# Kernel optimization log

Hardware: AMD Instinct MI355X
Metric: run time of the kernel (lower is better)

Reference implementation:

```python
import jax, jax.numpy as jnp
import numpy as np

N = 100_000      # num_nodes
E = 1_600_000    # num_edges (avg degree 16)
D = 64           # embedding_dim
L = 3            # num_layers


def setup_inputs() -> dict:
    key = jax.random.key(0)
    k1, k2 = jax.random.split(key)
    edge_index = jax.random.randint(k1, (2, E), 0, N, dtype=jnp.int64)
    edge_weight = jnp.ones((E,), jnp.float32)
    # nn.init.normal_(std=0.1)
    embedding = 0.1 * jax.random.normal(k2, (N, D), dtype=jnp.float32)
    return {"embedding": embedding, "edge_weight": edge_weight, "edge_index": edge_index}


def reference(embedding, edge_weight, edge_index):
    n = embedding.shape[0]
    self_idx = jnp.arange(n, dtype=edge_index.dtype)
    # add_self_loops: append (i, i) with weight 1 (PyG default fill_value)
    row = jnp.concatenate([edge_index[0], self_idx])  # source j
    col = jnp.concatenate([edge_index[1], self_idx])  # target i
    ew = jnp.concatenate([edge_weight, jnp.ones((n,), embedding.dtype)])
    # degree() counts occurrences of row (unweighted)
    deg = jax.ops.segment_sum(jnp.ones_like(ew), row, num_segments=n)
    deg_inv_sqrt = jnp.where(deg > 0, jax.lax.rsqrt(deg), 0.0)
    norm = deg_inv_sqrt[row] * ew * deg_inv_sqrt[col]  # [E+N]

    x = embedding
    acc = embedding  # running sum of layer-0..L embeddings
    for _ in range(L):
        # gather from source, scale, scatter-add to target (dropout off in eval)
        msg = norm[:, None] * x[row]                       # [E+N, D]
        x = jax.ops.segment_sum(msg, col, num_segments=n)  # [N, D]
        acc = acc + x
    return acc / (L + 1)
```

## Files before the change

### kernel.cpp

```cpp
#include <hip/hip_runtime.h>
#include <stdint.h>

#define DIM 64
#define BINS2 50000
#define RANGES 2
#define NSLICE 64
#define TBH 1024
#define SCAN_TILE 1024

__device__ __forceinline__ unsigned bf16rne(float f) {
    unsigned u = __float_as_uint(f);
    return (u + 0x7FFFu + ((u >> 16) & 1u)) >> 16;
}
__device__ __forceinline__ unsigned pack2(float lo, float hi) {
    return bf16rne(lo) | (bf16rne(hi) << 16);
}
#define UNPK(u, lo, hi) { lo = __uint_as_float((u) << 16); hi = __uint_as_float((u) & 0xFFFF0000u); }

__global__ void __launch_bounds__(TBH)
hist_kernel(const int* __restrict__ src, const int* __restrict__ dst,
            unsigned short* __restrict__ partialsA, unsigned short* __restrict__ partialsB,
            unsigned short* __restrict__ lrank, int E, int N, int Es) {
    __shared__ unsigned h32[BINS2 / 2];
    const int b = blockIdx.x;
    const int kind = b / (RANGES * NSLICE);
    const int rs = b % (RANGES * NSLICE);
    const int r = rs / NSLICE, s = rs % NSLICE;
    const int base = r * BINS2;
    const int hi = min(base + BINS2, N);
    const int nbw = (hi - base + 1) >> 1;
    for (int j = threadIdx.x; j < nbw; j += TBH) h32[j] = 0;
    __syncthreads();
    const int e0 = s * Es, e1 = min(e0 + Es, E);
    if (kind == 0) {
#pragma unroll 4
        for (int i = e0 + threadIdx.x; i < e1; i += TBH) {
            unsigned j = (unsigned)(dst[i] - base);
            if (j < (unsigned)BINS2) {
                const unsigned sh = (j & 1) * 16;
                unsigned old = atomicAdd(&h32[j >> 1], 1u << sh);
                lrank[i] = (unsigned short)((old >> sh) & 0xFFFFu);
            }
        }
    } else {
#pragma unroll 4
        for (int i = e0 + threadIdx.x; i < e1; i += TBH) {
            unsigned j = (unsigned)(src[i] - base);
            if (j < (unsigned)BINS2) atomicAdd(&h32[j >> 1], 1u << ((j & 1) * 16));
        }
    }
    __syncthreads();
    unsigned* part = (unsigned*)((kind ? partialsB : partialsA) + (size_t)s * N + base);
    for (int j = threadIdx.x; j < nbw; j += TBH) part[j] = h32[j];
}

__global__ void __launch_bounds__(256)
merge_kernel(unsigned short* __restrict__ partialsA, const unsigned short* __restrict__ partialsB,
             int* __restrict__ indeg, float* __restrict__ dis, int N) {
    const int i = blockIdx.x * blockDim.x + threadIdx.x;
    if (i >= N) return;
    int run = 0;
    for (int s = 0; s < NSLICE; ++s) {
        int v = partialsA[(size_t)s * N + i];
        partialsA[(size_t)s * N + i] = (unsigned short)run;
        run += v;
    }
    indeg[i] = run;
    int od = 0;
    for (int s = 0; s < NSLICE; ++s) od += partialsB[(size_t)s * N + i];
    dis[i] = rsqrtf((float)od + 1.0f);
}


__global__ void __launch_bounds__(256)
scan_partial(const int* __restrict__ indeg, int* __restrict__ partial, int n) {
    __shared__ int wsum[4];
    const int tid = threadIdx.x;
    const int base = blockIdx.x * SCAN_TILE + tid * 4;
    int s = 0;
    if (base + 3 < n) {
        int4 v = *(const int4*)(indeg + base);
        s = v.x + v.y + v.z + v.w;
    } else {
        for (int i = 0; i < 4; ++i) if (base + i < n) s += indeg[base + i];
    }
    for (int off = 32; off > 0; off >>= 1) s += __shfl_down(s, off, 64);
    const int lane = tid & 63, wid = tid >> 6;
    if (lane == 0) wsum[wid] = s;
    __syncthreads();
    if (tid == 0) partial[blockIdx.x] = wsum[0] + wsum[1] + wsum[2] + wsum[3];
}

__global__ void scan_blocksums(int* __restrict__ partial, int* __restrict__ offsets,
                               int nblocks, int n) {
    __shared__ int buf[1024];
    const int t = threadIdx.x;
    int v = (t < nblocks) ? partial[t] : 0;
    buf[t] = v;
    __syncthreads();
    for (int off = 1; off < 1024; off <<= 1) {
        int add = (t >= off) ? buf[t - off] : 0;
        __syncthreads();
        buf[t] += add;
        __syncthreads();
    }
    if (t < nblocks) partial[t] = buf[t] - v;
    if (t == 1023) offsets[n] = buf[1023];
}

__global__ void __launch_bounds__(256)
scan_final(const int* __restrict__ indeg, const int* __restrict__ partial,
           int* __restrict__ offsets, int n) {
    __shared__ int wpre[4];
    const int tid = threadIdx.x;
    const int base = blockIdx.x * SCAN_TILE + tid * 4;
    int v0 = 0, v1 = 0, v2 = 0, v3 = 0;
    if (base + 3 < n) {
        int4 v = *(const int4*)(indeg + base);
        v0 = v.x; v1 = v.y; v2 = v.z; v3 = v.w;
    } else {
        if (base + 0 < n) v0 = indeg[base + 0];
        if (base + 1 < n) v1 = indeg[base + 1];
        if (base + 2 < n) v2 = indeg[base + 2];
        if (base + 3 < n) v3 = indeg[base + 3];
    }
    const int s = v0 + v1 + v2 + v3;
    int inc = s;
    const int lane = tid & 63, wid = tid >> 6;
    for (int off = 1; off < 64; off <<= 1) {
        int t = __shfl_up(inc, off, 64);
        if (lane >= off) inc += t;
    }
    if (lane == 63) wpre[wid] = inc;
    __syncthreads();
    if (tid == 0) {
        int r = 0;
        for (int w = 0; w < 4; ++w) { int t = wpre[w]; wpre[w] = r; r += t; }
    }
    __syncthreads();
    int run = (inc - s) + wpre[wid] + partial[blockIdx.x];
    if (base + 0 < n) { offsets[base + 0] = run; run += v0; }
    if (base + 1 < n) { offsets[base + 1] = run; run += v1; }
    if (base + 2 < n) { offsets[base + 2] = run; run += v2; }
    if (base + 3 < n) { offsets[base + 3] = run; run += v3; }
}

__global__ void __launch_bounds__(256)
fill_kernel(const int* __restrict__ src, const int* __restrict__ dst,
            const float* __restrict__ ew, const float* __restrict__ dis,
            const int* __restrict__ offsets, const unsigned short* __restrict__ sliceoff,
            const unsigned short* __restrict__ lrank, int2* __restrict__ csr,
            int E, int N, int Es) {
    const int i0 = (blockIdx.x * blockDim.x + threadIdx.x) * 4;
    if (i0 + 3 < E) {
        int4   ss = *(const int4*)(src + i0);
        int4   tt = *(const int4*)(dst + i0);
        float4 ww = *(const float4*)(ew + i0);
        ushort4 lr = *(const ushort4*)(lrank + i0);
        int sl = i0 / Es;
#define DO(K, SF, TF, WF, LF) { int sE = (i0 + K) / Es; \
        int slot = offsets[TF] + sliceoff[(size_t)sE * N + TF] + (int)(LF); \
        csr[slot] = make_int2(SF, __float_as_int(dis[SF] * (WF) * dis[TF])); }
        (void)sl;
        DO(0, ss.x, tt.x, ww.x, lr.x)
        DO(1, ss.y, tt.y, ww.y, lr.y)
        DO(2, ss.z, tt.z, ww.z, lr.z)
        DO(3, ss.w, tt.w, ww.w, lr.w)
#undef DO
    } else {
        for (int i = i0; i < E; ++i) {
            int sE = i / Es;
            int t = dst[i], sc = src[i];
            float w = dis[sc] * ew[i] * dis[t];
            int slot = offsets[t] + sliceoff[(size_t)sE * N + t] + (int)lrank[i];
            csr[slot] = make_int2(sc, __float_as_int(w));
        }
    }
}

__global__ void __launch_bounds__(256)
conv_kernel(const float4* __restrict__ in4, uint4* __restrict__ outb, int n8) {
    int i = blockIdx.x * blockDim.x + threadIdx.x;
    if (i >= n8) return;
    float4 a = in4[2 * i], b = in4[2 * i + 1];
    uint4 o;
    o.x = pack2(a.x, a.y); o.y = pack2(a.z, a.w);
    o.z = pack2(b.x, b.y); o.w = pack2(b.z, b.w);
    outb[i] = o;
}

__global__ void __launch_bounds__(256)
prop_kernel(const uint4* __restrict__ xg, const float4* __restrict__ emb4,
            uint4* __restrict__ xstore, float4* __restrict__ out4,
            const int* __restrict__ offsets, const int2* __restrict__ csr,
            const float* __restrict__ dis, int n, int mode) {
    const int lane = threadIdx.x & 63;
    const int fl  = lane & 7;
    const int sub = lane >> 3;
    const int wave = blockIdx.x * (blockDim.x >> 6) + (threadIdx.x >> 6);
    const int node = wave * 8 + sub;
    if (node >= n) return;

    const int beg = offsets[node];
    const int end = offsets[node + 1];
    const float d = dis[node];
    const float dd = d * d;

    float a0, a1, a2, a3, a4, a5, a6, a7;
    float4 s0, s1;
    if (mode == 0) {
        s0 = emb4[node * 16 + fl * 2];
        s1 = emb4[node * 16 + fl * 2 + 1];
        a0 = dd * s0.x; a1 = dd * s0.y; a2 = dd * s0.z; a3 = dd * s0.w;
        a4 = dd * s1.x; a5 = dd * s1.y; a6 = dd * s1.z; a7 = dd * s1.w;
    } else {
        uint4 q = xg[(size_t)node * 8 + fl];
        float l, h;
        UNPK(q.x, l, h) a0 = dd * l; a1 = dd * h;
        UNPK(q.y, l, h) a2 = dd * l; a3 = dd * h;
        UNPK(q.z, l, h) a4 = dd * l; a5 = dd * h;
        UNPK(q.w, l, h) a6 = dd * l; a7 = dd * h;
    }

#define EDGE(E, Q) { float w_ = __int_as_float((E).y); float l, h; \
    UNPK((Q).x, l, h) a0 = fmaf(w_, l, a0); a1 = fmaf(w_, h, a1); \
    UNPK((Q).y, l, h) a2 = fmaf(w_, l, a2); a3 = fmaf(w_, h, a3); \
    UNPK((Q).z, l, h) a4 = fmaf(w_, l, a4); a5 = fmaf(w_, h, a5); \
    UNPK((Q).w, l, h) a6 = fmaf(w_, l, a6); a7 = fmaf(w_, h, a7); }

    int p = beg;
    for (; p + 4 <= end; p += 4) {
        int2 e0 = csr[p + 0], e1 = csr[p + 1], e2 = csr[p + 2], e3 = csr[p + 3];
        uint4 q0 = xg[(size_t)e0.x * 8 + fl];
        uint4 q1 = xg[(size_t)e1.x * 8 + fl];
        uint4 q2 = xg[(size_t)e2.x * 8 + fl];
        uint4 q3 = xg[(size_t)e3.x * 8 + fl];
        EDGE(e0, q0) EDGE(e1, q1) EDGE(e2, q2) EDGE(e3, q3)
    }
    for (; p < end; ++p) {
        int2 e = csr[p];
        uint4 q = xg[(size_t)e.x * 8 + fl];
        EDGE(e, q)
    }
#undef EDGE

    if (mode != 2) {
        uint4 o;
        o.x = pack2(a0, a1); o.y = pack2(a2, a3);
        o.z = pack2(a4, a5); o.w = pack2(a6, a7);
        xstore[(size_t)node * 8 + fl] = o;
    }
    const int oi = node * 16 + fl * 2;
    if (mode == 0) {
        out4[oi]     = make_float4(0.25f * (s0.x + a0), 0.25f * (s0.y + a1),
                                   0.25f * (s0.z + a2), 0.25f * (s0.w + a3));
        out4[oi + 1] = make_float4(0.25f * (s1.x + a4), 0.25f * (s1.y + a5),
                                   0.25f * (s1.z + a6), 0.25f * (s1.w + a7));
    } else {
        float4 p0 = out4[oi], p1 = out4[oi + 1];
        out4[oi]     = make_float4(fmaf(0.25f, a0, p0.x), fmaf(0.25f, a1, p0.y),
                                   fmaf(0.25f, a2, p0.z), fmaf(0.25f, a3, p0.w));
        out4[oi + 1] = make_float4(fmaf(0.25f, a4, p1.x), fmaf(0.25f, a5, p1.y),
                                   fmaf(0.25f, a6, p1.z), fmaf(0.25f, a7, p1.w));
    }
}


extern "C" void kernel_launch(void* const* d_in, const int* in_sizes, int n_in,
                              void* d_out, int out_size, void* d_ws, size_t ws_size,
                              hipStream_t stream) {
    const float* emb = (const float*)d_in[0];
    const float* ew  = (const float*)d_in[1];
    const int*   ei  = (const int*)d_in[2];
    const int E = in_sizes[2] / 2;
    const int N = in_sizes[0] / DIM;
    const int* src = ei;
    const int* dst = ei + E;
    float* out = (float*)d_out;

    const int Es = (E + NSLICE - 1) / NSLICE;
    const int nscan = (N + SCAN_TILE - 1) / SCAN_TILE;

    char* w = (char*)d_ws;
    unsigned short* partialsA = (unsigned short*)w; w += (size_t)NSLICE * N * 2;
    size_t unionSz = (size_t)NSLICE * N * 2;
    size_t xbSz = (size_t)N * DIM * 2;
    if (xbSz > unionSz) unionSz = xbSz;
    unionSz = (unionSz + 255) & ~(size_t)255;
    unsigned short* partialsB = (unsigned short*)w;
    uint4* xb = (uint4*)w; w += unionSz;
    unsigned short* lrank = (unsigned short*)w; w += (size_t)E * 2;
    int* indeg   = (int*)w;  w += (size_t)N * 4;
    int* offsets = (int*)w;  w += (size_t)(N + 1) * 4;
    float* dis   = (float*)w; w += (size_t)N * 4;
    int* partial = (int*)w;  w += (size_t)1024 * 4;
    w = (char*)(((uintptr_t)w + 255) & ~(uintptr_t)255);
    int2* csr    = (int2*)w; w += (size_t)E * 8;
    w = (char*)(((uintptr_t)w + 255) & ~(uintptr_t)255);
    uint4* x0c   = (uint4*)w; w += (size_t)N * DIM * 2;
    uint4* xa    = (uint4*)w; w += (size_t)N * DIM * 2;

    const int TB = 256;
    hist_kernel<<<2 * RANGES * NSLICE, TBH, 0, stream>>>(src, dst, partialsA, partialsB,
                                                         lrank, E, N, Es);
    merge_kernel<<<(N + TB - 1) / TB, TB, 0, stream>>>(partialsA, partialsB,
                                                       indeg, dis, N);
    scan_partial<<<nscan, TB, 0, stream>>>(indeg, partial, N);
    scan_blocksums<<<1, 1024, 0, stream>>>(partial, offsets, nscan, N);
    scan_final<<<nscan, TB, 0, stream>>>(indeg, partial, offsets, N);
    const int e4 = (E + 3) / 4;
    fill_kernel<<<(e4 + TB - 1) / TB, TB, 0, stream>>>(src, dst, ew, dis, offsets,
                                                       partialsA, lrank, csr, E, N, Es);
    const int n8 = N * DIM / 8;
    conv_kernel<<<(n8 + TB - 1) / TB, TB, 0, stream>>>((const float4*)emb, x0c, n8);

    dim3 grid((N + 31) / 32), block(TB);
    prop_kernel<<<grid, block, 0, stream>>>(x0c, (const float4*)emb, xa, (float4*)out,
                                            offsets, csr, dis, N, 0);
    prop_kernel<<<grid, block, 0, stream>>>(xa, nullptr, xb, (float4*)out,
                                            offsets, csr, dis, N, 1);
    prop_kernel<<<grid, block, 0, stream>>>(xb, nullptr, nullptr, (float4*)out,
                                            offsets, csr, dis, N, 2);
}
```

Before: 285.3 us.

## Replace direct CSR scatter with two-pass radix partition by destination range

The single fill kernel, which scattered each edge straight to its CSR slot through random offsets and sliceoff lookups, is replaced by a coarse partition pass. Edges are counted per destination range (2048 nodes) per edge slice, scanned, and written into a 16-byte-per-edge staging buffer grouped by range. A place kernel then writes CSR entries range by range, so offset, sliceoff and csr accesses stay local to a small node window and cache better. The cost is extra kernel launches, a serial single-block scan, and an extra read and write of the 16-byte staging buffer, which shares workspace memory with the bf16 feature buffers.

Result: slower. 303.3 us (+6.3%).

```diff
diff --git a/kernel.cpp b/kernel.cpp
--- a/kernel.cpp
+++ b/kernel.cpp
@@ -7,6 +7,9 @@
 #define NSLICE 64
 #define TBH 1024
 #define SCAN_TILE 1024
+#define PSLICE 256
+#define RSHIFT 11
+#define PB_G 8
 
 __device__ __forceinline__ unsigned bf16rne(float f) {
     unsigned u = __float_as_uint(f);
@@ -145,36 +148,74 @@
     if (base + 3 < n) { offsets[base + 3] = run; run += v3; }
 }
 
-__global__ void __launch_bounds__(256)
-fill_kernel(const int* __restrict__ src, const int* __restrict__ dst,
-            const float* __restrict__ ew, const float* __restrict__ dis,
-            const int* __restrict__ offsets, const unsigned short* __restrict__ sliceoff,
-            const unsigned short* __restrict__ lrank, int2* __restrict__ csr,
-            int E, int N, int Es) {
-    const int i0 = (blockIdx.x * blockDim.x + threadIdx.x) * 4;
-    if (i0 + 3 < E) {
-        int4   ss = *(const int4*)(src + i0);
-        int4   tt = *(const int4*)(dst + i0);
-        float4 ww = *(const float4*)(ew + i0);
-        ushort4 lr = *(const ushort4*)(lrank + i0);
-        int sl = i0 / Es;
-#define DO(K, SF, TF, WF, LF) { int sE = (i0 + K) / Es; \
-        int slot = offsets[TF] + sliceoff[(size_t)sE * N + TF] + (int)(LF); \
-        csr[slot] = make_int2(SF, __float_as_int(dis[SF] * (WF) * dis[TF])); }
-        (void)sl;
-        DO(0, ss.x, tt.x, ww.x, lr.x)
-        DO(1, ss.y, tt.y, ww.y, lr.y)
-        DO(2, ss.z, tt.z, ww.z, lr.z)
-        DO(3, ss.w, tt.w, ww.w, lr.w)
-#undef DO
-    } else {
-        for (int i = i0; i < E; ++i) {
-            int sE = i / Es;
-            int t = dst[i], sc = src[i];
-            float w = dis[sc] * ew[i] * dis[t];
-            int slot = offsets[t] + sliceoff[(size_t)sE * N + t] + (int)lrank[i];
-            csr[slot] = make_int2(sc, __float_as_int(w));
-        }
+
+__global__ void __launch_bounds__(256)
+count_part(const int* __restrict__ dst, int* __restrict__ cnt, int E, int Esp, int NR) {
+    __shared__ int c[64];
+    const int p = blockIdx.x;
+    if (threadIdx.x < 64) c[threadIdx.x] = 0;
+    __syncthreads();
+    const int e0 = p * Esp, e1 = min(e0 + Esp, E);
+    for (int i = e0 + threadIdx.x; i < e1; i += 256)
+        atomicAdd(&c[dst[i] >> RSHIFT], 1);
+    __syncthreads();
+    if (threadIdx.x < NR) cnt[threadIdx.x * PSLICE + p] = c[threadIdx.x];
+}
+
+__global__ void scan_part(const int* __restrict__ cnt, int* __restrict__ pscan, int n) {
+    __shared__ int buf[1024];
+    const int t = threadIdx.x;
+    const int chunk = (n + 1023) / 1024;
+    const int b0 = t * chunk, b1 = min(b0 + chunk, n);
+    int s = 0;
+    for (int i = b0; i < b1; ++i) s += cnt[i];
+    buf[t] = s;
+    __syncthreads();
+    for (int off = 1; off < 1024; off <<= 1) {
+        int add = (t >= off) ? buf[t - off] : 0;
+        __syncthreads();
+        buf[t] += add;
+        __syncthreads();
+    }
+    int run = buf[t] - s;
+    for (int i = b0; i < b1; ++i) { pscan[i] = run; run += cnt[i]; }
+    if (t == 1023) pscan[n] = buf[1023];
+}
+
+__global__ void __launch_bounds__(256)
+part_kernel(const int* __restrict__ src, const int* __restrict__ dst,
+            const float* __restrict__ ew, const unsigned short* __restrict__ lrank,
+            const float* __restrict__ dis, const int* __restrict__ pscan,
+            int4* __restrict__ part, int E, int Esp, int Esh, int NR) {
+    __shared__ int cur[64];
+    const int p = blockIdx.x;
+    if (threadIdx.x < NR) cur[threadIdx.x] = pscan[threadIdx.x * PSLICE + p];
+    __syncthreads();
+    const int e0 = p * Esp, e1 = min(e0 + Esp, E);
+    for (int i = e0 + threadIdx.x; i < e1; i += 256) {
+        int t = dst[i], sc = src[i];
+        float w = dis[sc] * ew[i] * dis[t];
+        int sh = i / Esh;
+        int pos = atomicAdd(&cur[t >> RSHIFT], 1);
+        part[pos] = make_int4(sc, t, __float_as_int(w), (sh << 24) | (int)lrank[i]);
+    }
+}
+
+__global__ void __launch_bounds__(256)
+place_kernel(const int4* __restrict__ part, const int* __restrict__ pscan,
+             const int* __restrict__ offsets, const unsigned short* __restrict__ sliceoff,
+             int2* __restrict__ csr, int N) {
+    const int r = blockIdx.x / PB_G;
+    const int g = blockIdx.x % PB_G;
+    const int idx0 = r * PSLICE + g * (PSLICE / PB_G);
+    const int start = pscan[idx0];
+    const int end = pscan[idx0 + PSLICE / PB_G];
+    for (int j = start + threadIdx.x; j < end; j += 256) {
+        int4 e = part[j];
+        int sh = ((unsigned)e.w) >> 24;
+        int lr = e.w & 0x00FFFFFF;
+        int slot = offsets[e.y] + sliceoff[(size_t)sh * N + e.y] + lr;
+        csr[slot] = make_int2(e.x, e.z);
     }
 }
 
@@ -278,7 +319,9 @@
     const int* dst = ei + E;
     float* out = (float*)d_out;
 
-    const int Es = (E + NSLICE - 1) / NSLICE;
+    const int Esh = (E + NSLICE - 1) / NSLICE;
+    const int Esp = (E + PSLICE - 1) / PSLICE;
+    const int NR  = (N + (1 << RSHIFT) - 1) >> RSHIFT;
     const int nscan = (N + SCAN_TILE - 1) / SCAN_TILE;
 
     char* w = (char*)d_ws;
@@ -294,23 +337,35 @@
     int* offsets = (int*)w;  w += (size_t)(N + 1) * 4;
     float* dis   = (float*)w; w += (size_t)N * 4;
     int* partial = (int*)w;  w += (size_t)1024 * 4;
+    int* cnt     = (int*)w;  w += (size_t)64 * PSLICE * 4;
+    int* pscan   = (int*)w;  w += ((size_t)64 * PSLICE + 1) * 4;
     w = (char*)(((uintptr_t)w + 255) & ~(uintptr_t)255);
     int2* csr    = (int2*)w; w += (size_t)E * 8;
     w = (char*)(((uintptr_t)w + 255) & ~(uintptr_t)255);
-    uint4* x0c   = (uint4*)w; w += (size_t)N * DIM * 2;
-    uint4* xa    = (uint4*)w; w += (size_t)N * DIM * 2;
+    size_t xSz = (size_t)N * DIM * 2;
+    size_t partSz = (size_t)E * 16;
+    size_t bigSz = (2 * xSz > partSz) ? 2 * xSz : partSz;
+    int4*  part  = (int4*)w;
+    uint4* x0c   = (uint4*)w;
+    uint4* xa    = (uint4*)(w + xSz);
+    w += (bigSz + 255) & ~(size_t)255;
 
     const int TB = 256;
     hist_kernel<<<2 * RANGES * NSLICE, TBH, 0, stream>>>(src, dst, partialsA, partialsB,
-                                                         lrank, E, N, Es);
+                                                         lrank, E, N, Esh);
     merge_kernel<<<(N + TB - 1) / TB, TB, 0, stream>>>(partialsA, partialsB,
                                                        indeg, dis, N);
     scan_partial<<<nscan, TB, 0, stream>>>(indeg, partial, N);
     scan_blocksums<<<1, 1024, 0, stream>>>(partial, offsets, nscan, N);
     scan_final<<<nscan, TB, 0, stream>>>(indeg, partial, offsets, N);
-    const int e4 = (E + 3) / 4;
-    fill_kernel<<<(e4 + TB - 1) / TB, TB, 0, stream>>>(src, dst, ew, dis, offsets,
-                                                       partialsA, lrank, csr, E, N, Es);
+
+    count_part<<<PSLICE, TB, 0, stream>>>(dst, cnt, E, Esp, NR);
+    scan_part<<<1, 1024, 0, stream>>>(cnt, pscan, NR * PSLICE);
+    part_kernel<<<PSLICE, TB, 0, stream>>>(src, dst, ew, lrank, dis, pscan,
+                                           part, E, Esp, Esh, NR);
+    place_kernel<<<NR * PB_G, TB, 0, stream>>>(part, pscan, offsets, partialsA,
+                                               csr, N);
+
     const int n8 = N * DIM / 8;
     conv_kernel<<<(n8 + TB - 1) / TB, TB, 0, stream>>>((const float4*)emb, x0c, n8);
 
```

## Defer output accumulation to a combine kernel and unroll edge gathers by eight

Applied to the files above, without the earlier changes.

Each propagation layer now only writes its bf16 result. A new combine kernel sums the fp32 embedding and the three bf16 layer outputs into the final output. This replaces the per-layer fp32 read-modify-write of the output buffer with one pass, at the cost of an extra launch and storing a third bf16 layer buffer (xc, aliased with the histogram partials). The neighbor gather loop also gains an 8-wide unrolled stage to keep more loads in flight, which adds register pressure.

Measured after the change: 284.8 us. Within noise of the previous version (-0.2%).

```diff
diff --git a/kernel.cpp b/kernel.cpp
--- a/kernel.cpp
+++ b/kernel.cpp
@@ -157,11 +157,9 @@
         int4   tt = *(const int4*)(dst + i0);
         float4 ww = *(const float4*)(ew + i0);
         ushort4 lr = *(const ushort4*)(lrank + i0);
-        int sl = i0 / Es;
 #define DO(K, SF, TF, WF, LF) { int sE = (i0 + K) / Es; \
         int slot = offsets[TF] + sliceoff[(size_t)sE * N + TF] + (int)(LF); \
         csr[slot] = make_int2(SF, __float_as_int(dis[SF] * (WF) * dis[TF])); }
-        (void)sl;
         DO(0, ss.x, tt.x, ww.x, lr.x)
         DO(1, ss.y, tt.y, ww.y, lr.y)
         DO(2, ss.z, tt.z, ww.z, lr.z)
@@ -190,10 +188,10 @@
 }
 
 __global__ void __launch_bounds__(256)
-prop_kernel(const uint4* __restrict__ xg, const float4* __restrict__ emb4,
-            uint4* __restrict__ xstore, float4* __restrict__ out4,
+prop_kernel(const uint4* __restrict__ xg, const float4* __restrict__ selfF,
+            uint4* __restrict__ xstore,
             const int* __restrict__ offsets, const int2* __restrict__ csr,
-            const float* __restrict__ dis, int n, int mode) {
+            const float* __restrict__ dis, int n) {
     const int lane = threadIdx.x & 63;
     const int fl  = lane & 7;
     const int sub = lane >> 3;
@@ -207,10 +205,9 @@
     const float dd = d * d;
 
     float a0, a1, a2, a3, a4, a5, a6, a7;
-    float4 s0, s1;
-    if (mode == 0) {
-        s0 = emb4[node * 16 + fl * 2];
-        s1 = emb4[node * 16 + fl * 2 + 1];
+    if (selfF) {
+        float4 s0 = selfF[node * 16 + fl * 2];
+        float4 s1 = selfF[node * 16 + fl * 2 + 1];
         a0 = dd * s0.x; a1 = dd * s0.y; a2 = dd * s0.z; a3 = dd * s0.w;
         a4 = dd * s1.x; a5 = dd * s1.y; a6 = dd * s1.z; a7 = dd * s1.w;
     } else {
@@ -229,6 +226,20 @@
     UNPK((Q).w, l, h) a6 = fmaf(w_, l, a6); a7 = fmaf(w_, h, a7); }
 
     int p = beg;
+    for (; p + 8 <= end; p += 8) {
+        int2 e0 = csr[p + 0], e1 = csr[p + 1], e2 = csr[p + 2], e3 = csr[p + 3];
+        int2 e4 = csr[p + 4], e5 = csr[p + 5], e6 = csr[p + 6], e7 = csr[p + 7];
+        uint4 q0 = xg[(size_t)e0.x * 8 + fl];
+        uint4 q1 = xg[(size_t)e1.x * 8 + fl];
+        uint4 q2 = xg[(size_t)e2.x * 8 + fl];
+        uint4 q3 = xg[(size_t)e3.x * 8 + fl];
+        uint4 q4 = xg[(size_t)e4.x * 8 + fl];
+        uint4 q5 = xg[(size_t)e5.x * 8 + fl];
+        uint4 q6 = xg[(size_t)e6.x * 8 + fl];
+        uint4 q7 = xg[(size_t)e7.x * 8 + fl];
+        EDGE(e0, q0) EDGE(e1, q1) EDGE(e2, q2) EDGE(e3, q3)
+        EDGE(e4, q4) EDGE(e5, q5) EDGE(e6, q6) EDGE(e7, q7)
+    }
     for (; p + 4 <= end; p += 4) {
         int2 e0 = csr[p + 0], e1 = csr[p + 1], e2 = csr[p + 2], e3 = csr[p + 3];
         uint4 q0 = xg[(size_t)e0.x * 8 + fl];
@@ -244,25 +255,36 @@
     }
 #undef EDGE
 
-    if (mode != 2) {
-        uint4 o;
-        o.x = pack2(a0, a1); o.y = pack2(a2, a3);
-        o.z = pack2(a4, a5); o.w = pack2(a6, a7);
-        xstore[(size_t)node * 8 + fl] = o;
-    }
-    const int oi = node * 16 + fl * 2;
-    if (mode == 0) {
-        out4[oi]     = make_float4(0.25f * (s0.x + a0), 0.25f * (s0.y + a1),
-                                   0.25f * (s0.z + a2), 0.25f * (s0.w + a3));
-        out4[oi + 1] = make_float4(0.25f * (s1.x + a4), 0.25f * (s1.y + a5),
-                                   0.25f * (s1.z + a6), 0.25f * (s1.w + a7));
-    } else {
-        float4 p0 = out4[oi], p1 = out4[oi + 1];
-        out4[oi]     = make_float4(fmaf(0.25f, a0, p0.x), fmaf(0.25f, a1, p0.y),
-                                   fmaf(0.25f, a2, p0.z), fmaf(0.25f, a3, p0.w));
-        out4[oi + 1] = make_float4(fmaf(0.25f, a4, p1.x), fmaf(0.25f, a5, p1.y),
-                                   fmaf(0.25f, a6, p1.z), fmaf(0.25f, a7, p1.w));
-    }
+    uint4 o;
+    o.x = pack2(a0, a1); o.y = pack2(a2, a3);
+    o.z = pack2(a4, a5); o.w = pack2(a6, a7);
+    xstore[(size_t)node * 8 + fl] = o;
+}
+
+__global__ void __launch_bounds__(256)
+combine_kernel(const float4* __restrict__ emb4, const uint4* __restrict__ xa,
+               const uint4* __restrict__ xb, const uint4* __restrict__ xc,
+               float4* __restrict__ out4, int n8) {
+    int i = blockIdx.x * blockDim.x + threadIdx.x;
+    if (i >= n8) return;
+    float4 e0 = emb4[2 * i], e1 = emb4[2 * i + 1];
+    uint4 qa = xa[i], qb = xb[i], qc = xc[i];
+    float r[8] = { e0.x, e0.y, e0.z, e0.w, e1.x, e1.y, e1.z, e1.w };
+    float l, h;
+    UNPK(qa.x, l, h) r[0] += l; r[1] += h;
+    UNPK(qa.y, l, h) r[2] += l; r[3] += h;
+    UNPK(qa.z, l, h) r[4] += l; r[5] += h;
+    UNPK(qa.w, l, h) r[6] += l; r[7] += h;
+    UNPK(qb.x, l, h) r[0] += l; r[1] += h;
+    UNPK(qb.y, l, h) r[2] += l; r[3] += h;
+    UNPK(qb.z, l, h) r[4] += l; r[5] += h;
+    UNPK(qb.w, l, h) r[6] += l; r[7] += h;
+    UNPK(qc.x, l, h) r[0] += l; r[1] += h;
+    UNPK(qc.y, l, h) r[2] += l; r[3] += h;
+    UNPK(qc.z, l, h) r[4] += l; r[5] += h;
+    UNPK(qc.w, l, h) r[6] += l; r[7] += h;
+    out4[2 * i]     = make_float4(0.25f * r[0], 0.25f * r[1], 0.25f * r[2], 0.25f * r[3]);
+    out4[2 * i + 1] = make_float4(0.25f * r[4], 0.25f * r[5], 0.25f * r[6], 0.25f * r[7]);
 }
 
 
@@ -282,13 +304,13 @@
     const int nscan = (N + SCAN_TILE - 1) / SCAN_TILE;
 
     char* w = (char*)d_ws;
-    unsigned short* partialsA = (unsigned short*)w; w += (size_t)NSLICE * N * 2;
-    size_t unionSz = (size_t)NSLICE * N * 2;
-    size_t xbSz = (size_t)N * DIM * 2;
-    if (xbSz > unionSz) unionSz = xbSz;
-    unionSz = (unionSz + 255) & ~(size_t)255;
+    size_t partSz = ((size_t)NSLICE * N * 2 + 255) & ~(size_t)255;
+    size_t xSz    = ((size_t)N * DIM * 2 + 255) & ~(size_t)255;
+    size_t uSz    = (partSz > xSz) ? partSz : xSz;
+    unsigned short* partialsA = (unsigned short*)w;
+    uint4* xc = (uint4*)w; w += uSz;
     unsigned short* partialsB = (unsigned short*)w;
-    uint4* xb = (uint4*)w; w += unionSz;
+    uint4* xb = (uint4*)w; w += uSz;
     unsigned short* lrank = (unsigned short*)w; w += (size_t)E * 2;
     int* indeg   = (int*)w;  w += (size_t)N * 4;
     int* offsets = (int*)w;  w += (size_t)(N + 1) * 4;
@@ -297,8 +319,8 @@
     w = (char*)(((uintptr_t)w + 255) & ~(uintptr_t)255);
     int2* csr    = (int2*)w; w += (size_t)E * 8;
     w = (char*)(((uintptr_t)w + 255) & ~(uintptr_t)255);
-    uint4* x0c   = (uint4*)w; w += (size_t)N * DIM * 2;
-    uint4* xa    = (uint4*)w; w += (size_t)N * DIM * 2;
+    uint4* x0c   = (uint4*)w; w += xSz;
+    uint4* xa    = (uint4*)w; w += xSz;
 
     const int TB = 256;
     hist_kernel<<<2 * RANGES * NSLICE, TBH, 0, stream>>>(src, dst, partialsA, partialsB,
@@ -315,10 +337,12 @@
     conv_kernel<<<(n8 + TB - 1) / TB, TB, 0, stream>>>((const float4*)emb, x0c, n8);
 
     dim3 grid((N + 31) / 32), block(TB);
-    prop_kernel<<<grid, block, 0, stream>>>(x0c, (const float4*)emb, xa, (float4*)out,
-                                            offsets, csr, dis, N, 0);
-    prop_kernel<<<grid, block, 0, stream>>>(xa, nullptr, xb, (float4*)out,
-                                            offsets, csr, dis, N, 1);
-    prop_kernel<<<grid, block, 0, stream>>>(xb, nullptr, nullptr, (float4*)out,
-                                            offsets, csr, dis, N, 2);
-}
+    prop_kernel<<<grid, block, 0, stream>>>(x0c, (const float4*)emb, xa,
+                                            offsets, csr, dis, N);
+    prop_kernel<<<grid, block, 0, stream>>>(xa, nullptr, xb,
+                                            offsets, csr, dis, N);
+    prop_kernel<<<grid, block, 0, stream>>>(xb, nullptr, xc,
+                                            offsets, csr, dis, N);
+    combine_kernel<<<(n8 + TB - 1) / TB, TB, 0, stream>>>((const float4*)emb, xa, xb, xc,
+                                                          (float4*)out, n8);
+}
```
